# Performance work log

Measured on AMD Instinct MI355X. Metric: run time of the kernel, lower is better.

## Reference

```python
import jax, jax.numpy as jnp
import numpy as np

KEY_DIM, VALUE_DIM, N_ACTIONS = 128, 64, 256
B, L = 32, 2048


def setup_inputs() -> dict:
    key = jax.random.key(0)
    k1, k2, k3 = jax.random.split(key, 3)
    key_vectors = jax.random.normal(k1, (B, L, KEY_DIM), dtype=jnp.float32)
    value_vectors = jax.random.normal(k2, (B, N_ACTIONS, KEY_DIM), dtype=jnp.float32)
    weights = jax.random.normal(k3, (KEY_DIM, VALUE_DIM, N_ACTIONS), dtype=jnp.float32)
    return {"key_vectors": key_vectors, "value_vectors": value_vectors, "weights": weights}


def reference(key_vectors, value_vectors, weights):
    # torch: einsum('bln,nka->bla', key, W) sums over both n (key_dim) and k (value_dim)
    scores = jnp.einsum('bln,nka->bla', key_vectors, weights)  # (B, L, A)
    # fused multiply-then-reduce over actions == batched matmul (no (B,L,A,D) intermediate)
    mem_vectors = jnp.einsum('bla,bad->bld', scores, value_vectors)  # (B, L, key_dim)
    q_values = jnp.einsum('bln,bmn->blm', key_vectors, mem_vectors)  # (B, L, L)
    return q_values
```

## Files before the change

### kernel.cpp

```cpp
#include <hip/hip_runtime.h>
#include <hip/hip_bf16.h>

#define KD 128
#define VD 64
#define NA 256
#define NB 32
#define LL 2048

typedef __attribute__((ext_vector_type(8))) short bf16x8;
typedef __attribute__((ext_vector_type(4))) float f32x4;
typedef __attribute__((ext_vector_type(8))) unsigned short u16x8;
typedef __attribute__((ext_vector_type(4))) unsigned short u16x4;

static __device__ __forceinline__ unsigned short f2bf(float x) {
  __hip_bfloat16 h = __float2bfloat16(x);
  unsigned short u;
  __builtin_memcpy(&u, &h, 2);
  return u;
}

static __device__ __forceinline__ void stage16(const void* gsrc, void* ldst) {
  __builtin_amdgcn_global_load_lds(
      (const __attribute__((address_space(1))) void*)gsrc,
      (__attribute__((address_space(3))) void*)ldst, 16, 0, 0);
}

__global__ __launch_bounds__(256) void fold_w(const float* __restrict__ W,
                                              float* __restrict__ W2) {
  const int idx = blockIdx.x * 256 + threadIdx.x;
  const int n = idx >> 8, a = idx & 255;
  const float* p = W + (long)n * (VD * NA) + a;
  float s = 0.f;
  #pragma unroll
  for (int k = 0; k < VD; ++k) s += p[k * NA];
  W2[idx] = s;
}

__global__ __launch_bounds__(128) void compute_t(const float* __restrict__ W2,
                                                 const float* __restrict__ V,
                                                 unsigned short* __restrict__ Tt) {
  const int n = threadIdx.x;
  const int d0 = blockIdx.x * 8;
  const int b = blockIdx.y;
  const float* vb = V + (long)b * NA * KD + d0;
  const float* w2p = W2 + n * NA;
  float acc[8] = {0.f, 0.f, 0.f, 0.f, 0.f, 0.f, 0.f, 0.f};
  for (int a = 0; a < NA; a += 4) {
    const float4 w = *(const float4*)(w2p + a);
    const float wq[4] = {w.x, w.y, w.z, w.w};
    #pragma unroll
    for (int q = 0; q < 4; ++q) {
      const float* vr = vb + (long)(a + q) * KD;
      #pragma unroll
      for (int j = 0; j < 8; ++j) acc[j] += wq[q] * vr[j];
    }
  }
  #pragma unroll
  for (int j = 0; j < 8; ++j)
    Tt[((long)b * KD + d0 + j) * KD + n] = f2bf(acc[j]);
}

__global__ __launch_bounds__(256) void cvt_key(const float* __restrict__ in,
                                               unsigned short* __restrict__ out) {
  const long i = ((long)blockIdx.x * 256 + threadIdx.x) * 8;
  const float4 f0 = *(const float4*)(in + i);
  const float4 f1 = *(const float4*)(in + i + 4);
  u16x8 r;
  r[0] = f2bf(f0.x); r[1] = f2bf(f0.y); r[2] = f2bf(f0.z); r[3] = f2bf(f0.w);
  r[4] = f2bf(f1.x); r[5] = f2bf(f1.y); r[6] = f2bf(f1.z); r[7] = f2bf(f1.w);
  *(u16x8*)(out + i) = r;
}

__global__ __launch_bounds__(256, 2) void gemm_q(const unsigned short* __restrict__ A,
                                                 const unsigned short* __restrict__ Tt,
                                                 float* __restrict__ C) {
  __shared__ unsigned short ldsB[16384];
  __shared__ unsigned short ldsA0[8192];
  __shared__ unsigned short ldsA1[8192];

  const int lg = (blockIdx.x & 7) * 64 + (blockIdx.x >> 3);
  const int nt = lg & 15;
  const int b = lg >> 4;

  const int tid = threadIdx.x;
  const int lane = tid & 63, w = tid >> 6;
  const int l15 = lane & 15, lhi = lane >> 4;
  const int wrM = w >> 1;
  const int wcN = w & 1;

  const unsigned short* gAb = A + (long)b * LL * KD;
  const unsigned short* gT = Tt + (long)b * KD * KD;
  const unsigned short* gChunk = gAb + (long)nt * 128 * KD;

  #pragma unroll
  for (int i = 0; i < 8; ++i) {
    const int addr = i * 4096 + tid * 16;
    const int row = addr >> 8;
    const int src = addr ^ ((row & 7) << 4);
    char* dst = (addr < 16384) ? ((char*)ldsA0 + addr) : ((char*)ldsA1 + addr - 16384);
    stage16((const char*)gT + src, dst);
    stage16((const char*)gChunk + src, (char*)ldsB + addr);
  }
  asm volatile("s_waitcnt vmcnt(0)" ::: "memory");
  __builtin_amdgcn_s_barrier();
  __builtin_amdgcn_sched_barrier(0);

  f32x4 pacc[2][8];
  #pragma unroll
  for (int i = 0; i < 2; ++i)
    #pragma unroll
    for (int j = 0; j < 8; ++j) pacc[i][j] = f32x4{0.f, 0.f, 0.f, 0.f};

  #pragma unroll
  for (int ks = 0; ks < 4; ++ks) {
    const int kb = (ks * 32 + lhi * 8) * 2;
    bf16x8 av[2], bv[8];
    #pragma unroll
    for (int rf = 0; rf < 2; ++rf) {
      const int row = w * 32 + rf * 16 + l15;
      const int byte = (row * 256 + kb) ^ ((row & 7) << 4);
      av[rf] = *(const bf16x8*)((const char*)ldsB + byte);
    }
    #pragma unroll
    for (int df = 0; df < 8; ++df) {
      const int row = df * 16 + l15;
      const int byte = (row * 256 + kb) ^ ((row & 7) << 4);
      bv[df] = (byte < 16384)
          ? *(const bf16x8*)((const char*)ldsA0 + byte)
          : *(const bf16x8*)((const char*)ldsA1 + (byte - 16384));
    }
    #pragma unroll
    for (int rf = 0; rf < 2; ++rf)
      #pragma unroll
      for (int df = 0; df < 8; ++df)
        pacc[rf][df] = __builtin_amdgcn_mfma_f32_16x16x32_bf16(bv[df], av[rf],
                                                               pacc[rf][df], 0, 0, 0);
  }
  asm volatile("s_waitcnt lgkmcnt(0)" ::: "memory");
  __builtin_amdgcn_sched_barrier(0);
  __builtin_amdgcn_s_barrier();
  __builtin_amdgcn_sched_barrier(0);

  #pragma unroll
  for (int i = 0; i < 4; ++i) {
    const int addr = i * 4096 + tid * 16;
    const int row = addr >> 8;
    const int src = addr ^ ((row & 7) << 4);
    stage16((const char*)gAb + src, (char*)ldsA0 + addr);
  }
  __builtin_amdgcn_sched_barrier(0);
  #pragma unroll
  for (int rf = 0; rf < 2; ++rf)
    #pragma unroll
    for (int df = 0; df < 8; ++df) {
      const int row = w * 32 + rf * 16 + l15;
      const int d = df * 16 + lhi * 4;
      u16x4 v;
      #pragma unroll
      for (int i = 0; i < 4; ++i) v[i] = f2bf(pacc[rf][df][i]);
      const int byte = (row * 256 + d * 2) ^ ((row & 7) << 4);
      *(u16x4*)((char*)ldsB + byte) = v;
    }
  asm volatile("s_waitcnt vmcnt(0) lgkmcnt(0)" ::: "memory");
  __builtin_amdgcn_sched_barrier(0);
  __builtin_amdgcn_s_barrier();
  __builtin_amdgcn_sched_barrier(0);

  const int col0 = nt * 128 + wcN * 64;

  auto gen = [&](int mt, const unsigned short* abuf, unsigned short* nbuf) {
    if (mt < 31) {
      const char* gA = (const char*)(gAb + (long)(mt + 1) * 64 * KD);
      #pragma unroll
      for (int i = 0; i < 4; ++i) {
        const int addr = i * 4096 + tid * 16;
        const int row = addr >> 8;
        const int src = addr ^ ((row & 7) << 4);
        stage16(gA + src, (char*)nbuf + addr);
      }
    }
    __builtin_amdgcn_sched_barrier(0);

    f32x4 acc[2][4];
    #pragma unroll
    for (int i = 0; i < 2; ++i)
      #pragma unroll
      for (int j = 0; j < 4; ++j) acc[i][j] = f32x4{0.f, 0.f, 0.f, 0.f};

    #pragma unroll
    for (int ks = 0; ks < 4; ++ks) {
      const int kb = (ks * 32 + lhi * 8) * 2;
      bf16x8 av[2], bv[4];
      #pragma unroll
      for (int mf = 0; mf < 2; ++mf) {
        const int row = wrM * 32 + mf * 16 + l15;
        const int byte = (row * 256 + kb) ^ ((row & 7) << 4);
        av[mf] = *(const bf16x8*)((const char*)abuf + byte);
      }
      #pragma unroll
      for (int nf = 0; nf < 4; ++nf) {
        const int row = wcN * 64 + nf * 16 + l15;
        const int byte = (row * 256 + kb) ^ ((row & 7) << 4);
        bv[nf] = *(const bf16x8*)((const char*)ldsB + byte);
      }
      #pragma unroll
      for (int mf = 0; mf < 2; ++mf)
        #pragma unroll
        for (int nf = 0; nf < 4; ++nf)
          acc[mf][nf] = __builtin_amdgcn_mfma_f32_16x16x32_bf16(bv[nf], av[mf],
                                                                acc[mf][nf], 0, 0, 0);
    }

    const long row0 = (long)b * LL + mt * 64 + wrM * 32;
    #pragma unroll
    for (int mf = 0; mf < 2; ++mf)
      #pragma unroll
      for (int nf = 0; nf < 4; ++nf) {
        const long r = row0 + mf * 16 + l15;
        const int c = col0 + nf * 16 + lhi * 4;
        *(f32x4*)(C + r * LL + c) = acc[mf][nf];
      }

    if (mt < 31) {
      asm volatile("s_waitcnt vmcnt(8)" ::: "memory");
      __builtin_amdgcn_sched_barrier(0);
      __builtin_amdgcn_s_barrier();
      __builtin_amdgcn_sched_barrier(0);
    }
  };

  #pragma unroll 1
  for (int mt2 = 0; mt2 < 16; ++mt2) {
    gen(2 * mt2, ldsA0, ldsA1);
    gen(2 * mt2 + 1, ldsA1, ldsA0);
  }
}

extern "C" void kernel_launch(void* const* d_in, const int* in_sizes, int n_in,
                              void* d_out, int out_size, void* d_ws, size_t ws_size,
                              hipStream_t stream) {
  const float* key = (const float*)d_in[0];
  const float* val = (const float*)d_in[1];
  const float* wts = (const float*)d_in[2];
  float* out = (float*)d_out;

  char* ws = (char*)d_ws;
  float* W2 = (float*)ws;
  unsigned short* Tt = (unsigned short*)(ws + 131072);
  unsigned short* keyB = (unsigned short*)(ws + 131072 + 1048576);

  fold_w<<<128, 256, 0, stream>>>(wts, W2);
  cvt_key<<<4096, 256, 0, stream>>>(key, keyB);
  compute_t<<<dim3(16, NB), 128, 0, stream>>>(W2, val, Tt);
  gemm_q<<<16 * NB, 256, 0, stream>>>(keyB, Tt, out);
}
```

Before: 172.3 us.

## Retile output GEMM to 512-thread blocks with 256-row key tiles

The main GEMM kernel grows from 4 to 8 waves per block. Each step now streams 256 key rows instead of 64, with double-buffered LDS of 64KB per buffer, so the outer loop runs 8 steps instead of 32 and needs far fewer barriers and staging rounds. Each wave now computes a 128x32 output slab instead of 32x64, and the prologue assigns one 16-row fragment per wave. Total LDS rises to about 160KB, which likely allows only one block per CU. Each wave's rows are also stored as narrower 128-byte segments, which may hurt write coalescing in a kernel dominated by output writes.

```diff
diff --git a/kernel.cpp b/kernel.cpp
--- a/kernel.cpp
+++ b/kernel.cpp
@@ -71,12 +71,12 @@
   *(u16x8*)(out + i) = r;
 }
 
-__global__ __launch_bounds__(256, 2) void gemm_q(const unsigned short* __restrict__ A,
+__global__ __launch_bounds__(512, 2) void gemm_q(const unsigned short* __restrict__ A,
                                                  const unsigned short* __restrict__ Tt,
                                                  float* __restrict__ C) {
   __shared__ unsigned short ldsB[16384];
-  __shared__ unsigned short ldsA0[8192];
-  __shared__ unsigned short ldsA1[8192];
+  __shared__ unsigned short ldsA0[32768];
+  __shared__ unsigned short ldsA1[32768];
 
   const int lg = (blockIdx.x & 7) * 64 + (blockIdx.x >> 3);
   const int nt = lg & 15;
@@ -85,56 +85,48 @@
   const int tid = threadIdx.x;
   const int lane = tid & 63, w = tid >> 6;
   const int l15 = lane & 15, lhi = lane >> 4;
-  const int wrM = w >> 1;
-  const int wcN = w & 1;
+  const int wrM = w >> 2;
+  const int wcN = w & 3;
 
   const unsigned short* gAb = A + (long)b * LL * KD;
   const unsigned short* gT = Tt + (long)b * KD * KD;
   const unsigned short* gChunk = gAb + (long)nt * 128 * KD;
 
   #pragma unroll
-  for (int i = 0; i < 8; ++i) {
-    const int addr = i * 4096 + tid * 16;
+  for (int i = 0; i < 4; ++i) {
+    const int addr = i * 8192 + tid * 16;
     const int row = addr >> 8;
     const int src = addr ^ ((row & 7) << 4);
-    char* dst = (addr < 16384) ? ((char*)ldsA0 + addr) : ((char*)ldsA1 + addr - 16384);
-    stage16((const char*)gT + src, dst);
+    stage16((const char*)gT + src, (char*)ldsA1 + addr);
     stage16((const char*)gChunk + src, (char*)ldsB + addr);
   }
   asm volatile("s_waitcnt vmcnt(0)" ::: "memory");
   __builtin_amdgcn_s_barrier();
   __builtin_amdgcn_sched_barrier(0);
 
-  f32x4 pacc[2][8];
-  #pragma unroll
-  for (int i = 0; i < 2; ++i)
-    #pragma unroll
-    for (int j = 0; j < 8; ++j) pacc[i][j] = f32x4{0.f, 0.f, 0.f, 0.f};
+  f32x4 pacc[8];
+  #pragma unroll
+  for (int j = 0; j < 8; ++j) pacc[j] = f32x4{0.f, 0.f, 0.f, 0.f};
 
   #pragma unroll
   for (int ks = 0; ks < 4; ++ks) {
     const int kb = (ks * 32 + lhi * 8) * 2;
-    bf16x8 av[2], bv[8];
-    #pragma unroll
-    for (int rf = 0; rf < 2; ++rf) {
-      const int row = w * 32 + rf * 16 + l15;
+    bf16x8 av, bv[8];
+    {
+      const int row = w * 16 + l15;
       const int byte = (row * 256 + kb) ^ ((row & 7) << 4);
-      av[rf] = *(const bf16x8*)((const char*)ldsB + byte);
+      av = *(const bf16x8*)((const char*)ldsB + byte);
     }
     #pragma unroll
     for (int df = 0; df < 8; ++df) {
       const int row = df * 16 + l15;
       const int byte = (row * 256 + kb) ^ ((row & 7) << 4);
-      bv[df] = (byte < 16384)
-          ? *(const bf16x8*)((const char*)ldsA0 + byte)
-          : *(const bf16x8*)((const char*)ldsA1 + (byte - 16384));
-    }
-    #pragma unroll
-    for (int rf = 0; rf < 2; ++rf)
-      #pragma unroll
-      for (int df = 0; df < 8; ++df)
-        pacc[rf][df] = __builtin_amdgcn_mfma_f32_16x16x32_bf16(bv[df], av[rf],
-                                                               pacc[rf][df], 0, 0, 0);
+      bv[df] = *(const bf16x8*)((const char*)ldsA1 + byte);
+    }
+    #pragma unroll
+    for (int df = 0; df < 8; ++df)
+      pacc[df] = __builtin_amdgcn_mfma_f32_16x16x32_bf16(bv[df], av,
+                                                         pacc[df], 0, 0, 0);
   }
   asm volatile("s_waitcnt lgkmcnt(0)" ::: "memory");
   __builtin_amdgcn_sched_barrier(0);
@@ -142,38 +134,36 @@
   __builtin_amdgcn_sched_barrier(0);
 
   #pragma unroll
-  for (int i = 0; i < 4; ++i) {
-    const int addr = i * 4096 + tid * 16;
+  for (int i = 0; i < 8; ++i) {
+    const int addr = i * 8192 + tid * 16;
     const int row = addr >> 8;
     const int src = addr ^ ((row & 7) << 4);
     stage16((const char*)gAb + src, (char*)ldsA0 + addr);
   }
   __builtin_amdgcn_sched_barrier(0);
   #pragma unroll
-  for (int rf = 0; rf < 2; ++rf)
-    #pragma unroll
-    for (int df = 0; df < 8; ++df) {
-      const int row = w * 32 + rf * 16 + l15;
-      const int d = df * 16 + lhi * 4;
-      u16x4 v;
-      #pragma unroll
-      for (int i = 0; i < 4; ++i) v[i] = f2bf(pacc[rf][df][i]);
-      const int byte = (row * 256 + d * 2) ^ ((row & 7) << 4);
-      *(u16x4*)((char*)ldsB + byte) = v;
-    }
+  for (int df = 0; df < 8; ++df) {
+    const int row = w * 16 + l15;
+    const int d = df * 16 + lhi * 4;
+    u16x4 v;
+    #pragma unroll
+    for (int i = 0; i < 4; ++i) v[i] = f2bf(pacc[df][i]);
+    const int byte = (row * 256 + d * 2) ^ ((row & 7) << 4);
+    *(u16x4*)((char*)ldsB + byte) = v;
+  }
   asm volatile("s_waitcnt vmcnt(0) lgkmcnt(0)" ::: "memory");
   __builtin_amdgcn_sched_barrier(0);
   __builtin_amdgcn_s_barrier();
   __builtin_amdgcn_sched_barrier(0);
 
-  const int col0 = nt * 128 + wcN * 64;
+  const int col0 = nt * 128 + wcN * 32;
 
   auto gen = [&](int mt, const unsigned short* abuf, unsigned short* nbuf) {
-    if (mt < 31) {
-      const char* gA = (const char*)(gAb + (long)(mt + 1) * 64 * KD);
-      #pragma unroll
-      for (int i = 0; i < 4; ++i) {
-        const int addr = i * 4096 + tid * 16;
+    if (mt < 7) {
+      const char* gA = (const char*)(gAb + (long)(mt + 1) * 256 * KD);
+      #pragma unroll
+      for (int i = 0; i < 8; ++i) {
+        const int addr = i * 8192 + tid * 16;
         const int row = addr >> 8;
         const int src = addr ^ ((row & 7) << 4);
         stage16(gA + src, (char*)nbuf + addr);
@@ -181,48 +171,48 @@
     }
     __builtin_amdgcn_sched_barrier(0);
 
-    f32x4 acc[2][4];
-    #pragma unroll
-    for (int i = 0; i < 2; ++i)
-      #pragma unroll
-      for (int j = 0; j < 4; ++j) acc[i][j] = f32x4{0.f, 0.f, 0.f, 0.f};
+    f32x4 acc[8][2];
+    #pragma unroll
+    for (int i = 0; i < 8; ++i)
+      #pragma unroll
+      for (int j = 0; j < 2; ++j) acc[i][j] = f32x4{0.f, 0.f, 0.f, 0.f};
 
     #pragma unroll
     for (int ks = 0; ks < 4; ++ks) {
       const int kb = (ks * 32 + lhi * 8) * 2;
-      bf16x8 av[2], bv[4];
-      #pragma unroll
-      for (int mf = 0; mf < 2; ++mf) {
-        const int row = wrM * 32 + mf * 16 + l15;
+      bf16x8 av[8], bv[2];
+      #pragma unroll
+      for (int mf = 0; mf < 8; ++mf) {
+        const int row = wrM * 128 + mf * 16 + l15;
         const int byte = (row * 256 + kb) ^ ((row & 7) << 4);
         av[mf] = *(const bf16x8*)((const char*)abuf + byte);
       }
       #pragma unroll
-      for (int nf = 0; nf < 4; ++nf) {
-        const int row = wcN * 64 + nf * 16 + l15;
+      for (int nf = 0; nf < 2; ++nf) {
+        const int row = wcN * 32 + nf * 16 + l15;
         const int byte = (row * 256 + kb) ^ ((row & 7) << 4);
         bv[nf] = *(const bf16x8*)((const char*)ldsB + byte);
       }
       #pragma unroll
-      for (int mf = 0; mf < 2; ++mf)
+      for (int mf = 0; mf < 8; ++mf)
         #pragma unroll
-        for (int nf = 0; nf < 4; ++nf)
+        for (int nf = 0; nf < 2; ++nf)
           acc[mf][nf] = __builtin_amdgcn_mfma_f32_16x16x32_bf16(bv[nf], av[mf],
                                                                 acc[mf][nf], 0, 0, 0);
     }
 
-    const long row0 = (long)b * LL + mt * 64 + wrM * 32;
-    #pragma unroll
-    for (int mf = 0; mf < 2; ++mf)
-      #pragma unroll
-      for (int nf = 0; nf < 4; ++nf) {
+    const long row0 = (long)b * LL + mt * 256 + wrM * 128;
+    #pragma unroll
+    for (int mf = 0; mf < 8; ++mf)
+      #pragma unroll
+      for (int nf = 0; nf < 2; ++nf) {
         const long r = row0 + mf * 16 + l15;
         const int c = col0 + nf * 16 + lhi * 4;
         *(f32x4*)(C + r * LL + c) = acc[mf][nf];
       }
 
-    if (mt < 31) {
-      asm volatile("s_waitcnt vmcnt(8)" ::: "memory");
+    if (mt < 7) {
+      asm volatile("s_waitcnt vmcnt(16)" ::: "memory");
       __builtin_amdgcn_sched_barrier(0);
       __builtin_amdgcn_s_barrier();
       __builtin_amdgcn_sched_barrier(0);
@@ -230,7 +220,7 @@
   };
 
   #pragma unroll 1
-  for (int mt2 = 0; mt2 < 16; ++mt2) {
+  for (int mt2 = 0; mt2 < 4; ++mt2) {
     gen(2 * mt2, ldsA0, ldsA1);
     gen(2 * mt2 + 1, ldsA1, ldsA0);
   }
@@ -252,5 +242,5 @@
   fold_w<<<128, 256, 0, stream>>>(wts, W2);
   cvt_key<<<4096, 256, 0, stream>>>(key, keyB);
   compute_t<<<dim3(16, NB), 128, 0, stream>>>(W2, val, Tt);
-  gemm_q<<<16 * NB, 256, 0, stream>>>(keyB, Tt, out);
-}
+  gemm_q<<<16 * NB, 512, 0, stream>>>(keyB, Tt, out);
+}
```

Result: faster. 153.9 us (-10.7%).

## Fuse fp32-to-bf16 key conversion into GEMM and widen tiles to 256 columns

Applied to the files above, without the earlier changes.

Removes the separate cvt_key kernel. The GEMM now stages fp32 key rows directly into LDS and converts them to bf16 fragments on the fly. The block is widened to 512 threads with 256 output columns per block, which halves the grid and the number of times each batch's key stream is re-read. In exchange, each A tile moves twice the bytes per row through LDS, adds per-fragment conversion work in the inner loop, and roughly doubles LDS use per block, which may reduce occupancy.

```diff
diff --git a/kernel.cpp b/kernel.cpp
--- a/kernel.cpp
+++ b/kernel.cpp
@@ -23,6 +23,15 @@
   __builtin_amdgcn_global_load_lds(
       (const __attribute__((address_space(1))) void*)gsrc,
       (__attribute__((address_space(3))) void*)ldst, 16, 0, 0);
+}
+
+static __device__ __forceinline__ bf16x8 frag_cvt(const f32x4 a, const f32x4 b) {
+  u16x8 v;
+  v[0] = f2bf(a[0]); v[1] = f2bf(a[1]); v[2] = f2bf(a[2]); v[3] = f2bf(a[3]);
+  v[4] = f2bf(b[0]); v[5] = f2bf(b[1]); v[6] = f2bf(b[2]); v[7] = f2bf(b[3]);
+  bf16x8 r;
+  __builtin_memcpy(&r, &v, 16);
+  return r;
 }
 
 __global__ __launch_bounds__(256) void fold_w(const float* __restrict__ W,
@@ -60,104 +69,106 @@
     Tt[((long)b * KD + d0 + j) * KD + n] = f2bf(acc[j]);
 }
 
-__global__ __launch_bounds__(256) void cvt_key(const float* __restrict__ in,
-                                               unsigned short* __restrict__ out) {
-  const long i = ((long)blockIdx.x * 256 + threadIdx.x) * 8;
-  const float4 f0 = *(const float4*)(in + i);
-  const float4 f1 = *(const float4*)(in + i + 4);
-  u16x8 r;
-  r[0] = f2bf(f0.x); r[1] = f2bf(f0.y); r[2] = f2bf(f0.z); r[3] = f2bf(f0.w);
-  r[4] = f2bf(f1.x); r[5] = f2bf(f1.y); r[6] = f2bf(f1.z); r[7] = f2bf(f1.w);
-  *(u16x8*)(out + i) = r;
-}
-
-__global__ __launch_bounds__(256, 2) void gemm_q(const unsigned short* __restrict__ A,
+__global__ __launch_bounds__(512, 2) void gemm_q(const float* __restrict__ key,
                                                  const unsigned short* __restrict__ Tt,
                                                  float* __restrict__ C) {
-  __shared__ unsigned short ldsB[16384];
-  __shared__ unsigned short ldsA0[8192];
-  __shared__ unsigned short ldsA1[8192];
-
-  const int lg = (blockIdx.x & 7) * 64 + (blockIdx.x >> 3);
-  const int nt = lg & 15;
-  const int b = lg >> 4;
+  __shared__ unsigned short ldsB[32768];
+  __shared__ float ldsA0[8192];
+  __shared__ float ldsA1[8192];
+
+  const int lg = (blockIdx.x & 7) * 32 + (blockIdx.x >> 3);
+  const int nt = lg & 7;
+  const int b = lg >> 3;
 
   const int tid = threadIdx.x;
   const int lane = tid & 63, w = tid >> 6;
   const int l15 = lane & 15, lhi = lane >> 4;
-  const int wrM = w >> 1;
-  const int wcN = w & 1;
-
-  const unsigned short* gAb = A + (long)b * LL * KD;
+  const int wrM = w >> 2;
+  const int wcN = w & 3;
+
+  const float* gK = key + (long)b * LL * KD;
   const unsigned short* gT = Tt + (long)b * KD * KD;
-  const unsigned short* gChunk = gAb + (long)nt * 128 * KD;
-
-  #pragma unroll
-  for (int i = 0; i < 8; ++i) {
-    const int addr = i * 4096 + tid * 16;
+  const float* gChunk = gK + (long)nt * 256 * KD;
+
+  #pragma unroll
+  for (int i = 0; i < 4; ++i) {
+    const int addr = i * 8192 + tid * 16;
     const int row = addr >> 8;
     const int src = addr ^ ((row & 7) << 4);
-    char* dst = (addr < 16384) ? ((char*)ldsA0 + addr) : ((char*)ldsA1 + addr - 16384);
-    stage16((const char*)gT + src, dst);
-    stage16((const char*)gChunk + src, (char*)ldsB + addr);
-  }
-  asm volatile("s_waitcnt vmcnt(0)" ::: "memory");
-  __builtin_amdgcn_s_barrier();
+    stage16((const char*)gT + src, (char*)ldsB + 32768 + addr);
+  }
+
+  f32x4 pacc[2][8];
+  #pragma unroll
+  for (int i = 0; i < 2; ++i)
+    #pragma unroll
+    for (int j = 0; j < 8; ++j) pacc[i][j] = f32x4{0.f, 0.f, 0.f, 0.f};
+
+  #pragma unroll 1
+  for (int h = 0; h < 2; ++h) {
+    const char* gsrc = (const char*)(gChunk + (long)h * 128 * KD);
+    #pragma unroll
+    for (int i = 0; i < 8; ++i) {
+      const int addr = i * 8192 + tid * 16;
+      const int row = addr >> 9;
+      const int src = addr ^ ((row & 7) << 4);
+      char* dst = (addr < 32768) ? ((char*)ldsA0 + addr) : ((char*)ldsA1 + addr - 32768);
+      stage16(gsrc + src, dst);
+    }
+    asm volatile("s_waitcnt vmcnt(0)" ::: "memory");
+    __builtin_amdgcn_s_barrier();
+    __builtin_amdgcn_sched_barrier(0);
+
+    #pragma unroll
+    for (int ks = 0; ks < 4; ++ks) {
+      const int kb = (ks * 32 + lhi * 8) * 2;
+      const int row = w * 16 + l15;
+      const int fb = (row * 512 + (ks * 32 + lhi * 8) * 4) ^ ((row & 7) << 4);
+      const int fbh = fb ^ 16;
+      f32x4 lo, hi;
+      if (fb < 32768) {
+        lo = *(const f32x4*)((const char*)ldsA0 + fb);
+        hi = *(const f32x4*)((const char*)ldsA0 + fbh);
+      } else {
+        lo = *(const f32x4*)((const char*)ldsA1 + fb - 32768);
+        hi = *(const f32x4*)((const char*)ldsA1 + fbh - 32768);
+      }
+      const bf16x8 av = frag_cvt(lo, hi);
+      bf16x8 bv[8];
+      #pragma unroll
+      for (int df = 0; df < 8; ++df) {
+        const int trow = df * 16 + l15;
+        const int byte = (trow * 256 + kb) ^ ((trow & 7) << 4);
+        bv[df] = *(const bf16x8*)((const char*)ldsB + 32768 + byte);
+      }
+      #pragma unroll
+      for (int df = 0; df < 8; ++df)
+        pacc[h][df] = __builtin_amdgcn_mfma_f32_16x16x32_bf16(bv[df], av,
+                                                              pacc[h][df], 0, 0, 0);
+    }
+    asm volatile("s_waitcnt lgkmcnt(0)" ::: "memory");
+    __builtin_amdgcn_sched_barrier(0);
+    __builtin_amdgcn_s_barrier();
+    __builtin_amdgcn_sched_barrier(0);
+  }
+
+  #pragma unroll
+  for (int i = 0; i < 4; ++i) {
+    const int addr = i * 8192 + tid * 16;
+    const int row = addr >> 9;
+    const int src = addr ^ ((row & 7) << 4);
+    stage16((const char*)gK + src, (char*)ldsA0 + addr);
+  }
   __builtin_amdgcn_sched_barrier(0);
-
-  f32x4 pacc[2][8];
-  #pragma unroll
-  for (int i = 0; i < 2; ++i)
-    #pragma unroll
-    for (int j = 0; j < 8; ++j) pacc[i][j] = f32x4{0.f, 0.f, 0.f, 0.f};
-
-  #pragma unroll
-  for (int ks = 0; ks < 4; ++ks) {
-    const int kb = (ks * 32 + lhi * 8) * 2;
-    bf16x8 av[2], bv[8];
-    #pragma unroll
-    for (int rf = 0; rf < 2; ++rf) {
-      const int row = w * 32 + rf * 16 + l15;
-      const int byte = (row * 256 + kb) ^ ((row & 7) << 4);
-      av[rf] = *(const bf16x8*)((const char*)ldsB + byte);
-    }
+  #pragma unroll
+  for (int h = 0; h < 2; ++h)
     #pragma unroll
     for (int df = 0; df < 8; ++df) {
-      const int row = df * 16 + l15;
-      const int byte = (row * 256 + kb) ^ ((row & 7) << 4);
-      bv[df] = (byte < 16384)
-          ? *(const bf16x8*)((const char*)ldsA0 + byte)
-          : *(const bf16x8*)((const char*)ldsA1 + (byte - 16384));
-    }
-    #pragma unroll
-    for (int rf = 0; rf < 2; ++rf)
-      #pragma unroll
-      for (int df = 0; df < 8; ++df)
-        pacc[rf][df] = __builtin_amdgcn_mfma_f32_16x16x32_bf16(bv[df], av[rf],
-                                                               pacc[rf][df], 0, 0, 0);
-  }
-  asm volatile("s_waitcnt lgkmcnt(0)" ::: "memory");
-  __builtin_amdgcn_sched_barrier(0);
-  __builtin_amdgcn_s_barrier();
-  __builtin_amdgcn_sched_barrier(0);
-
-  #pragma unroll
-  for (int i = 0; i < 4; ++i) {
-    const int addr = i * 4096 + tid * 16;
-    const int row = addr >> 8;
-    const int src = addr ^ ((row & 7) << 4);
-    stage16((const char*)gAb + src, (char*)ldsA0 + addr);
-  }
-  __builtin_amdgcn_sched_barrier(0);
-  #pragma unroll
-  for (int rf = 0; rf < 2; ++rf)
-    #pragma unroll
-    for (int df = 0; df < 8; ++df) {
-      const int row = w * 32 + rf * 16 + l15;
+      const int row = h * 128 + w * 16 + l15;
       const int d = df * 16 + lhi * 4;
       u16x4 v;
       #pragma unroll
-      for (int i = 0; i < 4; ++i) v[i] = f2bf(pacc[rf][df][i]);
+      for (int i = 0; i < 4; ++i) v[i] = f2bf(pacc[h][df][i]);
       const int byte = (row * 256 + d * 2) ^ ((row & 7) << 4);
       *(u16x4*)((char*)ldsB + byte) = v;
     }
@@ -166,15 +177,15 @@
   __builtin_amdgcn_s_barrier();
   __builtin_amdgcn_sched_barrier(0);
 
-  const int col0 = nt * 128 + wcN * 64;
-
-  auto gen = [&](int mt, const unsigned short* abuf, unsigned short* nbuf) {
+  const int col0 = nt * 256 + wcN * 64;
+
+  auto gen = [&](int mt, const float* abuf, float* nbuf) {
     if (mt < 31) {
-      const char* gA = (const char*)(gAb + (long)(mt + 1) * 64 * KD);
+      const char* gA = (const char*)(gK + (long)(mt + 1) * 64 * KD);
       #pragma unroll
       for (int i = 0; i < 4; ++i) {
-        const int addr = i * 4096 + tid * 16;
-        const int row = addr >> 8;
+        const int addr = i * 8192 + tid * 16;
+        const int row = addr >> 9;
         const int src = addr ^ ((row & 7) << 4);
         stage16(gA + src, (char*)nbuf + addr);
       }
@@ -194,8 +205,10 @@
       #pragma unroll
       for (int mf = 0; mf < 2; ++mf) {
         const int row = wrM * 32 + mf * 16 + l15;
-        const int byte = (row * 256 + kb) ^ ((row & 7) << 4);
-        av[mf] = *(const bf16x8*)((const char*)abuf + byte);
+        const int fb = (row * 512 + (ks * 32 + lhi * 8) * 4) ^ ((row & 7) << 4);
+        const f32x4 lo = *(const f32x4*)((const char*)abuf + fb);
+        const f32x4 hi = *(const f32x4*)((const char*)abuf + (fb ^ 16));
+        av[mf] = frag_cvt(lo, hi);
       }
       #pragma unroll
       for (int nf = 0; nf < 4; ++nf) {
@@ -247,10 +260,8 @@
   char* ws = (char*)d_ws;
   float* W2 = (float*)ws;
   unsigned short* Tt = (unsigned short*)(ws + 131072);
-  unsigned short* keyB = (unsigned short*)(ws + 131072 + 1048576);
 
   fold_w<<<128, 256, 0, stream>>>(wts, W2);
-  cvt_key<<<4096, 256, 0, stream>>>(key, keyB);
   compute_t<<<dim3(16, NB), 128, 0, stream>>>(W2, val, Tt);
-  gemm_q<<<16 * NB, 256, 0, stream>>>(keyB, Tt, out);
-}
+  gemm_q<<<8 * NB, 512, 0, stream>>>(key, Tt, out);
+}
```

Measured after the change: 201.1 us. +16.7%, slower.
